# Optimization experiments

Hardware: AMD Instinct MI355X
Metric: run time of the kernel (lower is better)

## Reference

```python
import jax, jax.numpy as jnp
import numpy as np
import math

N_EMBD = 768
N_HEAD = 12
B, T = 4, 2048
HEAD_DIM = N_EMBD // N_HEAD


def new_gelu(x):
    # GPT-2 tanh approximation of GELU (NewGELUActivation)
    c = math.sqrt(2.0 / math.pi)
    return 0.5 * x * (1.0 + jnp.tanh(c * (x + 0.044715 * jnp.power(x, 3.0))))


def layer_norm(x, g, b, eps=1e-5):
    mu = jnp.mean(x, axis=-1, keepdims=True)
    var = jnp.mean(jnp.square(x - mu), axis=-1, keepdims=True)
    return (x - mu) * jax.lax.rsqrt(var + eps) * g + b


def setup_inputs() -> dict:
    key = jax.random.key(0)
    ks = jax.random.split(key, 12)
    s = 0.02
    return {
        "x": jax.random.normal(ks[0], (B, T, N_EMBD), dtype=jnp.float32),
        "ln1_g": jnp.ones((N_EMBD,), jnp.float32),
        "ln1_b": jnp.zeros((N_EMBD,), jnp.float32),
        "W_attn": jax.random.normal(ks[1], (N_EMBD, 3 * N_EMBD), jnp.float32) * s,
        "b_attn": jnp.zeros((3 * N_EMBD,), jnp.float32),
        "W_proj": jax.random.normal(ks[2], (N_EMBD, N_EMBD), jnp.float32) * s,
        "b_proj": jnp.zeros((N_EMBD,), jnp.float32),
        "ln2_g": jnp.ones((N_EMBD,), jnp.float32),
        "ln2_b": jnp.zeros((N_EMBD,), jnp.float32),
        "W_fc": jax.random.normal(ks[3], (N_EMBD, 4 * N_EMBD), jnp.float32) * s,
        "b_fc": jnp.zeros((4 * N_EMBD,), jnp.float32),
        "W_fc2": jax.random.normal(ks[4], (4 * N_EMBD, N_EMBD), jnp.float32) * s,
        "b_fc2": jnp.zeros((N_EMBD,), jnp.float32),
    }


def block_forward(x, ln1_g, ln1_b, W_attn, b_attn, W_proj, b_proj,
                  ln2_g, ln2_b, W_fc, b_fc, W_fc2, b_fc2):
    # ---- attention sublayer (pre-LN) ----
    h = layer_norm(x, ln1_g, ln1_b)
    qkv = h @ W_attn + b_attn                      # [B,T,3C]
    q, k, v = jnp.split(qkv, 3, axis=-1)
    q = q.reshape(B, T, N_HEAD, HEAD_DIM).transpose(0, 2, 1, 3)  # [B,H,T,D]
    k = k.reshape(B, T, N_HEAD, HEAD_DIM).transpose(0, 2, 1, 3)
    v = v.reshape(B, T, N_HEAD, HEAD_DIM).transpose(0, 2, 1, 3)
    scores = jnp.einsum('bhqd,bhkd->bhqk', q, k) / math.sqrt(HEAD_DIM)
    causal = jnp.tril(jnp.ones((T, T), dtype=bool))
    scores = jnp.where(causal[None, None, :, :], scores, -jnp.inf)
    attn = jax.nn.softmax(scores, axis=-1)
    y = jnp.einsum('bhqk,bhkd->bhqd', attn, v)      # [B,H,T,D]
    y = y.transpose(0, 2, 1, 3).reshape(B, T, N_EMBD)
    y = y @ W_proj + b_proj
    x = x + y
    # ---- MLP sublayer ----
    h = layer_norm(x, ln2_g, ln2_b)
    h = new_gelu(h @ W_fc + b_fc)
    h = h @ W_fc2 + b_fc2
    return x + h


def reference(x, ln1_g, ln1_b, W_attn, b_attn, W_proj, b_proj,
              ln2_g, ln2_b, W_fc, b_fc, W_fc2, b_fc2):
    return block_forward(x, ln1_g, ln1_b, W_attn, b_attn, W_proj, b_proj,
                         ln2_g, ln2_b, W_fc, b_fc, W_fc2, b_fc2)
```

## Files before the change

kernel.cpp:

```cpp
#include <hip/hip_runtime.h>
#include <hip/hip_bf16.h>

typedef __attribute__((ext_vector_type(8))) short short8;
typedef __attribute__((ext_vector_type(4))) float f32x4;
typedef __attribute__((ext_vector_type(8))) unsigned short u16x8;
typedef __attribute__((ext_vector_type(4))) unsigned short u16x4;

#define MFMA16(A, B, C) __builtin_amdgcn_mfma_f32_16x16x32_bf16(A, B, C, 0, 0, 0)

static __device__ __forceinline__ unsigned short f2bf(float f) {
    unsigned int u = __builtin_bit_cast(unsigned int, f);
    u += 0x7FFF + ((u >> 16) & 1);
    return (unsigned short)(u >> 16);
}

static __device__ __forceinline__ float bf2f(unsigned short u) {
    return __builtin_bit_cast(float, (unsigned int)u << 16);
}

static __device__ __forceinline__ unsigned int cvt_pk_bf16(float a, float b) {
    unsigned int r;
    asm("v_cvt_pk_bf16_f32 %0, %1, %2" : "=v"(r) : "v"(a), "v"(b));
    return r;
}

static __device__ __forceinline__ float gelu_f(float v) {
    const float k1 = 2.3022077646f;
    const float k2 = 0.1029432207f;
    float t = __builtin_amdgcn_exp2f(-(k1 * v + k2 * v * v * v));
    return v * __builtin_amdgcn_rcpf(1.0f + t);
}

typedef const __attribute__((address_space(1))) unsigned int* gas_t;
typedef __attribute__((address_space(3))) unsigned int* las_t;
static __device__ __forceinline__ void gl_lds16(const void* g, void* l) {
    __builtin_amdgcn_global_load_lds((gas_t)g, (las_t)l, 16, 0, 0);
}

__global__ __launch_bounds__(256)
void wtrans_all(const float* __restrict__ W0, const float* __restrict__ W1,
                const float* __restrict__ W2, const float* __restrict__ W3,
                unsigned short* __restrict__ T0, unsigned short* __restrict__ T1,
                unsigned short* __restrict__ T2, unsigned short* __restrict__ T3) {
    __shared__ float tl[32][33];
    const int idx = blockIdx.x;
    const float* W; unsigned short* Wt; int K, N, nx, bx;
    if (idx < 1728)      { W = W0; Wt = T0; K = 768;  N = 2304; bx = idx;        nx = 72; }
    else if (idx < 2304) { W = W1; Wt = T1; K = 768;  N = 768;  bx = idx - 1728; nx = 24; }
    else if (idx < 4608) { W = W2; Wt = T2; K = 768;  N = 3072; bx = idx - 2304; nx = 96; }
    else                 { W = W3; Wt = T3; K = 3072; N = 768;  bx = idx - 4608; nx = 24; }
    const int n0 = (bx % nx) * 32, k0 = (bx / nx) * 32;
    const int tx = threadIdx.x & 31, ty = threadIdx.x >> 5;
#pragma unroll
    for (int i = 0; i < 4; i++)
        tl[ty + 8 * i][tx] = W[(long)(k0 + ty + 8 * i) * N + n0 + tx];
    __syncthreads();
#pragma unroll
    for (int i = 0; i < 4; i++)
        Wt[(long)(n0 + ty + 8 * i) * K + k0 + tx] = f2bf(tl[tx][ty + 8 * i]);
}

template <bool BF16IN>
__global__ __launch_bounds__(256)
void ln_fwd(const void* __restrict__ xin, const float* __restrict__ gw,
            const float* __restrict__ bw, unsigned short* __restrict__ out) {
    const int row = blockIdx.x * 4 + (threadIdx.x >> 6);
    const int ln = threadIdx.x & 63;
    float4 v[3];
    if constexpr (BF16IN) {
        const unsigned short* xr = (const unsigned short*)xin + (long)row * 768;
#pragma unroll
        for (int j = 0; j < 3; j++) {
            u16x4 t = *(const u16x4*)(xr + (ln + 64 * j) * 4);
            v[j].x = bf2f(t[0]); v[j].y = bf2f(t[1]);
            v[j].z = bf2f(t[2]); v[j].w = bf2f(t[3]);
        }
    } else {
        const float4* xr = (const float4*)((const float*)xin + (long)row * 768);
#pragma unroll
        for (int j = 0; j < 3; j++) v[j] = xr[ln + 64 * j];
    }
    float s = 0.f;
#pragma unroll
    for (int j = 0; j < 3; j++) s += v[j].x + v[j].y + v[j].z + v[j].w;
#pragma unroll
    for (int off = 32; off >= 1; off >>= 1) s += __shfl_xor(s, off);
    const float mean = s * (1.0f / 768.0f);
    float sq = 0.f;
#pragma unroll
    for (int j = 0; j < 3; j++) {
        float a = v[j].x - mean, b = v[j].y - mean, c = v[j].z - mean, d = v[j].w - mean;
        sq += a * a + b * b + c * c + d * d;
    }
#pragma unroll
    for (int off = 32; off >= 1; off >>= 1) sq += __shfl_xor(sq, off);
    const float rstd = rsqrtf(sq * (1.0f / 768.0f) + 1e-5f);
#pragma unroll
    for (int j = 0; j < 3; j++) {
        const int c = ln + 64 * j;
        float4 gg = ((const float4*)gw)[c];
        float4 bb = ((const float4*)bw)[c];
        u16x4 o;
        o[0] = f2bf((v[j].x - mean) * rstd * gg.x + bb.x);
        o[1] = f2bf((v[j].y - mean) * rstd * gg.y + bb.y);
        o[2] = f2bf((v[j].z - mean) * rstd * gg.z + bb.z);
        o[3] = f2bf((v[j].w - mean) * rstd * gg.w + bb.w);
        *(u16x4*)(out + (long)row * 768 + c * 4) = o;
    }
}

template <int MODE, int BN, int BM, int BK>
__global__ __launch_bounds__(BM * 2)
void gemm_bt(const unsigned short* __restrict__ A, const unsigned short* __restrict__ Bt,
             const float* __restrict__ bias, const void* __restrict__ resid,
             void* __restrict__ Out, unsigned short* __restrict__ vT,
             int M, int N, int K) {
    constexpr int NTH = BM * 2;
    constexpr int NW = BN / 32;
    constexpr int CHK = BK / 8;
    constexpr int BUF = (BM + BN) * BK;
    constexpr int RPP = NTH / CHK;
    constexpr int RPW = 64 / CHK;
    constexpr int PA = BM / RPP;
    constexpr int PB = BN / RPP;
    constexpr int STN = (BN == 128) ? 132 : 68;
    constexpr int SEGS = NTH / 64;
    constexpr int CPT = BN / SEGS;
    constexpr int BYTES_MAIN = 2 * BUF * 2;
    constexpr int BYTES_ST = 64 * STN * 4;
    constexpr int BYTES = BYTES_MAIN > BYTES_ST ? BYTES_MAIN : BYTES_ST;
    __shared__ char smem[BYTES];
    unsigned short* ubase = (unsigned short*)smem;
    float* st = (float*)smem;

    const int tid = threadIdx.x;
    const int wv = tid >> 6, ln = tid & 63;
    const int wm = wv >> 1, wn = wv & 1;
    const int g = ln >> 4, r = ln & 15;
    const int sr = ln / CHK, sc = ln % CHK;
    const int ssw = (BK == 32) ? (sc ^ ((sr >> 1) & 3)) : (sc ^ (sr & 7));
    const long mbase = (long)blockIdx.x * BM;
    const long nbase = (long)blockIdx.y * BN;

    f32x4 acc[4][NW];
    const f32x4 zero = {0.f, 0.f, 0.f, 0.f};
#pragma unroll
    for (int m = 0; m < 4; m++)
#pragma unroll
        for (int n = 0; n < NW; n++) acc[m][n] = zero;

    const int nt = K / BK;
#pragma unroll
    for (int p = 0; p < PA; p++)
        gl_lds16(A + (mbase + p * RPP + wv * RPW + sr) * (long)K + ssw * 8,
                 ubase + (p * RPP + wv * RPW) * BK);
#pragma unroll
    for (int p = 0; p < PB; p++)
        gl_lds16(Bt + (nbase + p * RPP + wv * RPW + sr) * (long)K + ssw * 8,
                 ubase + BM * BK + (p * RPP + wv * RPW) * BK);
    __syncthreads();

    const int cx = (r >> 1) & 3;
    const int rx = r & 7;
    for (int t = 0; t < nt; t++) {
        const unsigned short* cbuf = ubase + (t & 1) * BUF;
        if (t + 1 < nt) {
            unsigned short* nbuf = ubase + ((t + 1) & 1) * BUF;
            const long k0 = (long)(t + 1) * BK;
#pragma unroll
            for (int p = 0; p < PA; p++)
                gl_lds16(A + (mbase + p * RPP + wv * RPW + sr) * (long)K + k0 + ssw * 8,
                         nbuf + (p * RPP + wv * RPW) * BK);
#pragma unroll
            for (int p = 0; p < PB; p++)
                gl_lds16(Bt + (nbase + p * RPP + wv * RPW + sr) * (long)K + k0 + ssw * 8,
                         nbuf + BM * BK + (p * RPP + wv * RPW) * BK);
        }
        if constexpr (BK == 32) {
            short8 af[4], bfr[NW];
#pragma unroll
            for (int m = 0; m < 4; m++)
                af[m] = *(const short8*)(cbuf + (wm * 64 + m * 16 + r) * 32 + ((g ^ cx) * 8));
#pragma unroll
            for (int n = 0; n < NW; n++)
                bfr[n] = *(const short8*)(cbuf + BM * 32 + (wn * (BN / 2) + n * 16 + r) * 32 + ((g ^ cx) * 8));
#pragma unroll
            for (int m = 0; m < 4; m++)
#pragma unroll
                for (int n = 0; n < NW; n++) acc[m][n] = MFMA16(af[m], bfr[n], acc[m][n]);
        } else {
#pragma unroll
            for (int ks = 0; ks < 2; ks++) {
                short8 af[4], bfr[NW];
#pragma unroll
                for (int m = 0; m < 4; m++)
                    af[m] = *(const short8*)(cbuf + (wm * 64 + m * 16 + r) * 64 + (((g + 4 * ks) ^ rx) * 8));
#pragma unroll
                for (int n = 0; n < NW; n++)
                    bfr[n] = *(const short8*)(cbuf + BM * 64 + (wn * (BN / 2) + n * 16 + r) * 64 + (((g + 4 * ks) ^ rx) * 8));
#pragma unroll
                for (int m = 0; m < 4; m++)
#pragma unroll
                    for (int n = 0; n < NW; n++) acc[m][n] = MFMA16(af[m], bfr[n], acc[m][n]);
            }
        }
        __syncthreads();
    }

    const int tr = tid / SEGS, seg = tid % SEGS;
#pragma unroll 1
    for (int half = 0; half < BM / 64; half++) {
        __syncthreads();
        if (wm == half) {
#pragma unroll
            for (int m = 0; m < 4; m++)
#pragma unroll
                for (int n = 0; n < NW; n++)
#pragma unroll
                    for (int i = 0; i < 4; i++)
                        st[(m * 16 + g * 4 + i) * STN + wn * (BN / 2) + n * 16 + r] = acc[m][n][i];
        }
        __syncthreads();
        const long row = mbase + half * 64 + tr;
        if constexpr (MODE == 1) {
            if (nbase >= 1536) {
                constexpr int DC = NTH / 8;
                const int tc = tid & 7;
                const int d0 = tid >> 3;
                const long bb = mbase >> 11;
                const int tg0 = (int)(mbase & 2047) + half * 64 + tc * 8;
#pragma unroll
                for (int it = 0; it < 128 / DC; it++) {
                    const int dl = it * DC + d0;
                    const int h = (int)((nbase - 1536) >> 6) + (dl >> 6);
                    const int dd = dl & 63;
                    const float bc = bias[nbase + dl];
                    u16x8 o;
#pragma unroll
                    for (int j = 0; j < 8; j++)
                        o[j] = f2bf(st[(tc * 8 + j) * STN + dl] + bc);
                    *(u16x8*)(vT + ((bb * 12 + h) * 64 + dd) * 2048 + tg0) = o;
                }
            } else {
                const float qs = (nbase < 768) ? 0.18033688011112042f : 1.0f;
                const long cb = nbase + seg * CPT;
                unsigned short* op = (unsigned short*)Out + row * N + cb;
#pragma unroll
                for (int u2 = 0; u2 < CPT / 8; u2++) {
                    float4 a = *(const float4*)(st + tr * STN + seg * CPT + u2 * 8);
                    float4 b = *(const float4*)(st + tr * STN + seg * CPT + u2 * 8 + 4);
                    float4 ba = ((const float4*)bias)[(cb >> 2) + u2 * 2];
                    float4 bb2 = ((const float4*)bias)[(cb >> 2) + u2 * 2 + 1];
                    a.x = (a.x + ba.x) * qs; a.y = (a.y + ba.y) * qs;
                    a.z = (a.z + ba.z) * qs; a.w = (a.w + ba.w) * qs;
                    b.x = (b.x + bb2.x) * qs; b.y = (b.y + bb2.y) * qs;
                    b.z = (b.z + bb2.z) * qs; b.w = (b.w + bb2.w) * qs;
                    uint4 w;
                    w.x = cvt_pk_bf16(a.x, a.y);
                    w.y = cvt_pk_bf16(a.z, a.w);
                    w.z = cvt_pk_bf16(b.x, b.y);
                    w.w = cvt_pk_bf16(b.z, b.w);
                    *(uint4*)(op + u2 * 8) = w;
                }
            }
        } else if constexpr (MODE == 3) {
            const long cb = nbase + seg * CPT;
            unsigned short* op = (unsigned short*)Out + row * N + cb;
#pragma unroll
            for (int u2 = 0; u2 < CPT / 8; u2++) {
                float4 a = *(const float4*)(st + tr * STN + seg * CPT + u2 * 8);
                float4 b = *(const float4*)(st + tr * STN + seg * CPT + u2 * 8 + 4);
                float4 ba = ((const float4*)bias)[(cb >> 2) + u2 * 2];
                float4 bb2 = ((const float4*)bias)[(cb >> 2) + u2 * 2 + 1];
                a.x = gelu_f(a.x + ba.x); a.y = gelu_f(a.y + ba.y);
                a.z = gelu_f(a.z + ba.z); a.w = gelu_f(a.w + ba.w);
                b.x = gelu_f(b.x + bb2.x); b.y = gelu_f(b.y + bb2.y);
                b.z = gelu_f(b.z + bb2.z); b.w = gelu_f(b.w + bb2.w);
                uint4 w;
                w.x = cvt_pk_bf16(a.x, a.y);
                w.y = cvt_pk_bf16(a.z, a.w);
                w.z = cvt_pk_bf16(b.x, b.y);
                w.w = cvt_pk_bf16(b.z, b.w);
                *(uint4*)(op + u2 * 8) = w;
            }
        } else if constexpr (MODE == 2) {
            const long cb = nbase + seg * CPT;
            unsigned short* op = (unsigned short*)Out + row * N + cb;
            const float* rp = (const float*)resid + row * N + cb;
#pragma unroll
            for (int u2 = 0; u2 < CPT / 8; u2++) {
                float4 a = *(const float4*)(st + tr * STN + seg * CPT + u2 * 8);
                float4 b = *(const float4*)(st + tr * STN + seg * CPT + u2 * 8 + 4);
                float4 ba = ((const float4*)bias)[(cb >> 2) + u2 * 2];
                float4 bb2 = ((const float4*)bias)[(cb >> 2) + u2 * 2 + 1];
                float4 ra = ((const float4*)rp)[u2 * 2];
                float4 rb = ((const float4*)rp)[u2 * 2 + 1];
                a.x += ba.x + ra.x; a.y += ba.y + ra.y;
                a.z += ba.z + ra.z; a.w += ba.w + ra.w;
                b.x += bb2.x + rb.x; b.y += bb2.y + rb.y;
                b.z += bb2.z + rb.z; b.w += bb2.w + rb.w;
                uint4 w;
                w.x = cvt_pk_bf16(a.x, a.y);
                w.y = cvt_pk_bf16(a.z, a.w);
                w.z = cvt_pk_bf16(b.x, b.y);
                w.w = cvt_pk_bf16(b.z, b.w);
                *(uint4*)(op + u2 * 8) = w;
            }
        } else {
            const long cb = nbase + seg * CPT;
            float* op = (float*)Out + row * N + cb;
            const unsigned short* rp = (const unsigned short*)resid + row * N + cb;
#pragma unroll
            for (int u = 0; u < CPT / 4; u++) {
                float4 a = *(const float4*)(st + tr * STN + seg * CPT + u * 4);
                float4 ba = ((const float4*)bias)[(cb >> 2) + u];
                u16x4 rv = *(const u16x4*)(rp + u * 4);
                a.x += ba.x + bf2f(rv[0]); a.y += ba.y + bf2f(rv[1]);
                a.z += ba.z + bf2f(rv[2]); a.w += ba.w + bf2f(rv[3]);
                ((float4*)op)[u] = a;
            }
        }
    }
}

__global__ __launch_bounds__(256)
void attn_fwd(const unsigned short* __restrict__ qkv, const unsigned short* __restrict__ vT,
              unsigned short* __restrict__ y) {
    const int pair = blockIdx.x;
    const int bh = blockIdx.y;
    const int b = bh / 12, h = bh % 12;
    const int qtA = pair, qtB = 31 - pair;
    __shared__ unsigned short smem[2 * 64 * 64 + 2 * 64 * 64 + 64 * 64];
    unsigned short* Kl = smem;
    unsigned short* Vl = smem + 2 * 4096;
    unsigned short* Pl = smem + 4 * 4096;
    const int tid = threadIdx.x;
    const int wv = tid >> 6, ln = tid & 63;
    const int g = ln >> 4, r = ln & 15;
    const int lr = ln >> 3, l8 = ln & 7;
    const int sw = l8 ^ lr;
    const int rx = r & 7;
    const f32x4 zero = {0.f, 0.f, 0.f, 0.f};
    const int q = wv * 16 + r;

    const int q7 = q & 7;
    unsigned short* plw[4];
#pragma unroll
    for (int kf = 0; kf < 4; kf++)
        plw[kf] = Pl + q * 64 + ((2 * kf + (g >> 1)) ^ q7) * 8 + (g & 1) * 4;
    const unsigned short* plr0 = Pl + q * 64 + (g ^ q7) * 8;
    const unsigned short* plr1 = Pl + q * 64 + ((4 + g) ^ q7) * 8;

    const long qoffA = ((long)(b * 2048 + qtA * 64 + q)) * 2304 + h * 64;
    const long qoffB = ((long)(b * 2048 + qtB * 64 + q)) * 2304 + h * 64;
    short8 bqA0 = *(const short8*)(qkv + qoffA + g * 8);
    short8 bqA1 = *(const short8*)(qkv + qoffA + 32 + g * 8);
    short8 bqB0 = *(const short8*)(qkv + qoffB + g * 8);
    short8 bqB1 = *(const short8*)(qkv + qoffB + 32 + g * 8);

    float lA = 0.0f, lB = 0.0f;
    f32x4 oA[4], oB[4];
#pragma unroll
    for (int f = 0; f < 4; f++) { oA[f] = zero; oB[f] = zero; }

    auto process = [&](const short8& b0, const short8& b1, float& lrow,
                       f32x4* oacc, bool diag, const unsigned short* Kb,
                       const unsigned short* Vb) {
        f32x4 s[4];
#pragma unroll
        for (int kf = 0; kf < 4; kf++) {
            short8 a0 = *(const short8*)(Kb + (kf * 16 + r) * 64 + (g ^ rx) * 8);
            short8 a1 = *(const short8*)(Kb + (kf * 16 + r) * 64 + ((g + 4) ^ rx) * 8);
            s[kf] = MFMA16(a0, b0, zero);
            s[kf] = MFMA16(a1, b1, s[kf]);
        }
        if (diag) {
#pragma unroll
            for (int kf = 0; kf < 4; kf++)
#pragma unroll
                for (int i = 0; i < 4; i++)
                    if (kf * 16 + g * 4 + i > q) s[kf][i] = -1e30f;
        }
        float pv[4][4];
        float psum = 0.f;
#pragma unroll
        for (int kf = 0; kf < 4; kf++)
#pragma unroll
            for (int i = 0; i < 4; i++) {
                pv[kf][i] = __builtin_amdgcn_exp2f(s[kf][i]);
                psum += pv[kf][i];
            }
        psum += __shfl_xor(psum, 16);
        psum += __shfl_xor(psum, 32);
        lrow += psum;
#pragma unroll
        for (int kf = 0; kf < 4; kf++) {
            uint2 w;
            w.x = cvt_pk_bf16(pv[kf][0], pv[kf][1]);
            w.y = cvt_pk_bf16(pv[kf][2], pv[kf][3]);
            *(uint2*)plw[kf] = w;
        }
        short8 pb0 = *(const short8*)plr0;
        short8 pb1 = *(const short8*)plr1;
#pragma unroll
        for (int f = 0; f < 4; f++) {
            short8 va0 = *(const short8*)(Vb + (f * 16 + r) * 64 + (g ^ rx) * 8);
            short8 va1 = *(const short8*)(Vb + (f * 16 + r) * 64 + ((g + 4) ^ rx) * 8);
            oacc[f] = MFMA16(va0, pb0, oacc[f]);
            oacc[f] = MFMA16(va1, pb1, oacc[f]);
        }
    };

#pragma unroll
    for (int p = 0; p < 2; p++) {
        const int row = wv * 8 + p * 32 + lr;
        gl_lds16(qkv + ((long)(b * 2048 + row)) * 2304 + 768 + h * 64 + sw * 8,
                 (char*)Kl + (wv * 8 + p * 32) * 128);
        gl_lds16(vT + ((long)(bh * 64 + row)) * 2048 + sw * 8,
                 (char*)Vl + (wv * 8 + p * 32) * 128);
    }
    __syncthreads();

    for (int kt = 0; kt <= qtB; ++kt) {
        const unsigned short* Kb = Kl + (kt & 1) * 4096;
        const unsigned short* Vb = Vl + (kt & 1) * 4096;
        if (kt < qtB) {
            char* Kn = (char*)Kl + ((kt + 1) & 1) * 8192;
            char* Vn = (char*)Vl + ((kt + 1) & 1) * 8192;
#pragma unroll
            for (int p = 0; p < 2; p++) {
                const int row = wv * 8 + p * 32 + lr;
                gl_lds16(qkv + ((long)(b * 2048 + (kt + 1) * 64 + row)) * 2304 + 768 + h * 64 + sw * 8,
                         Kn + (wv * 8 + p * 32) * 128);
                gl_lds16(vT + ((long)(bh * 64 + row)) * 2048 + (kt + 1) * 64 + sw * 8,
                         Vn + (wv * 8 + p * 32) * 128);
            }
        }
        if (kt <= qtA) process(bqA0, bqA1, lA, oA, kt == qtA, Kb, Vb);
        process(bqB0, bqB1, lB, oB, kt == qtB, Kb, Vb);
        __syncthreads();
    }

#pragma unroll 1
    for (int e = 0; e < 2; e++) {
        const float inv = 1.0f / (e ? lB : lA);
        const f32x4* oacc = e ? oB : oA;
        const int q0 = (e ? qtB : qtA) * 64;
#pragma unroll
        for (int f = 0; f < 4; f++) {
            uint2 w;
            w.x = cvt_pk_bf16(oacc[f][0] * inv, oacc[f][1] * inv);
            w.y = cvt_pk_bf16(oacc[f][2] * inv, oacc[f][3] * inv);
            *(uint2*)plw[f] = w;
        }
        __syncthreads();
#pragma unroll
        for (int p = 0; p < 2; p++) {
            int idx = p * 256 + tid;
            int row = idx >> 3, cc = idx & 7;
            *(u16x8*)(y + ((long)(b * 2048 + q0 + row)) * 768 + h * 64 + cc * 8) =
                *(const u16x8*)(Pl + row * 64 + (cc ^ (row & 7)) * 8);
        }
        __syncthreads();
    }
}

extern "C" void kernel_launch(void* const* d_in, const int* in_sizes, int n_in,
                              void* d_out, int out_size, void* d_ws, size_t ws_size,
                              hipStream_t stream) {
    const float* x      = (const float*)d_in[0];
    const float* ln1_g  = (const float*)d_in[1];
    const float* ln1_b  = (const float*)d_in[2];
    const float* W_attn = (const float*)d_in[3];
    const float* b_attn = (const float*)d_in[4];
    const float* W_proj = (const float*)d_in[5];
    const float* b_proj = (const float*)d_in[6];
    const float* ln2_g  = (const float*)d_in[7];
    const float* ln2_b  = (const float*)d_in[8];
    const float* W_fc   = (const float*)d_in[9];
    const float* b_fc   = (const float*)d_in[10];
    const float* W_fc2  = (const float*)d_in[11];
    const float* b_fc2  = (const float*)d_in[12];

    char* ws = (char*)d_ws;
    size_t off = 0;
    auto alloc = [&](size_t bytes) -> char* {
        char* p = ws + off;
        off += (bytes + 255) & ~(size_t)255;
        return p;
    };
    unsigned short* WtA  = (unsigned short*)alloc((size_t)2304 * 768 * 2);
    unsigned short* WtP  = (unsigned short*)alloc((size_t)768 * 768 * 2);
    unsigned short* WtF  = (unsigned short*)alloc((size_t)3072 * 768 * 2);
    unsigned short* WtF2 = (unsigned short*)alloc((size_t)768 * 3072 * 2);
    unsigned short* bigA = (unsigned short*)alloc((size_t)8192 * 3072 * 2);
    unsigned short* x1   = (unsigned short*)alloc((size_t)8192 * 768 * 2);
    unsigned short* bufD = (unsigned short*)alloc((size_t)8192 * 768 * 2);
    unsigned short* vT   = (unsigned short*)alloc((size_t)48 * 64 * 2048 * 2);

    wtrans_all<<<6912, 256, 0, stream>>>(W_attn, W_proj, W_fc, W_fc2, WtA, WtP, WtF, WtF2);
    ln_fwd<false><<<2048, 256, 0, stream>>>(x, ln1_g, ln1_b, bufD);
    gemm_bt<1, 128, 256, 32><<<dim3(32, 18), 512, 0, stream>>>(bufD, WtA, b_attn, nullptr, bigA, vT, 8192, 2304, 768);
    attn_fwd<<<dim3(16, 48), 256, 0, stream>>>(bigA, vT, bufD);
    gemm_bt<2, 64, 128, 64><<<dim3(64, 12), 256, 0, stream>>>(bufD, WtP, b_proj, x, x1, nullptr, 8192, 768, 768);
    ln_fwd<true><<<2048, 256, 0, stream>>>(x1, ln2_g, ln2_b, bufD);
    gemm_bt<3, 128, 256, 32><<<dim3(32, 24), 512, 0, stream>>>(bufD, WtF, b_fc, nullptr, bigA, nullptr, 8192, 3072, 768);
    gemm_bt<4, 64, 128, 64><<<dim3(64, 12), 256, 0, stream>>>(bigA, WtF2, b_fc2, x1, (float*)d_out, nullptr, 8192, 768, 3072);
}
```

Before: 246.5 us.

## Fuse weight transpose with first LayerNorm and store K in per-head contiguous layout

```diff
diff --git a/kernel.cpp b/kernel.cpp
--- a/kernel.cpp
+++ b/kernel.cpp
@@ -38,47 +38,79 @@
 }
 
 __global__ __launch_bounds__(256)
-void wtrans_all(const float* __restrict__ W0, const float* __restrict__ W1,
-                const float* __restrict__ W2, const float* __restrict__ W3,
-                unsigned short* __restrict__ T0, unsigned short* __restrict__ T1,
-                unsigned short* __restrict__ T2, unsigned short* __restrict__ T3) {
+void prep_all(const float* __restrict__ W0, const float* __restrict__ W1,
+              const float* __restrict__ W2, const float* __restrict__ W3,
+              unsigned short* __restrict__ T0, unsigned short* __restrict__ T1,
+              unsigned short* __restrict__ T2, unsigned short* __restrict__ T3,
+              const float* __restrict__ x, const float* __restrict__ gw,
+              const float* __restrict__ bw, unsigned short* __restrict__ lnout) {
     __shared__ float tl[32][33];
     const int idx = blockIdx.x;
-    const float* W; unsigned short* Wt; int K, N, nx, bx;
-    if (idx < 1728)      { W = W0; Wt = T0; K = 768;  N = 2304; bx = idx;        nx = 72; }
-    else if (idx < 2304) { W = W1; Wt = T1; K = 768;  N = 768;  bx = idx - 1728; nx = 24; }
-    else if (idx < 4608) { W = W2; Wt = T2; K = 768;  N = 3072; bx = idx - 2304; nx = 96; }
-    else                 { W = W3; Wt = T3; K = 3072; N = 768;  bx = idx - 4608; nx = 24; }
-    const int n0 = (bx % nx) * 32, k0 = (bx / nx) * 32;
-    const int tx = threadIdx.x & 31, ty = threadIdx.x >> 5;
-#pragma unroll
-    for (int i = 0; i < 4; i++)
-        tl[ty + 8 * i][tx] = W[(long)(k0 + ty + 8 * i) * N + n0 + tx];
-    __syncthreads();
-#pragma unroll
-    for (int i = 0; i < 4; i++)
-        Wt[(long)(n0 + ty + 8 * i) * K + k0 + tx] = f2bf(tl[tx][ty + 8 * i]);
-}
-
-template <bool BF16IN>
+    if (idx < 6912) {
+        const float* W; unsigned short* Wt; int K, N, nx, bx;
+        if (idx < 1728)      { W = W0; Wt = T0; K = 768;  N = 2304; bx = idx;        nx = 72; }
+        else if (idx < 2304) { W = W1; Wt = T1; K = 768;  N = 768;  bx = idx - 1728; nx = 24; }
+        else if (idx < 4608) { W = W2; Wt = T2; K = 768;  N = 3072; bx = idx - 2304; nx = 96; }
+        else                 { W = W3; Wt = T3; K = 3072; N = 768;  bx = idx - 4608; nx = 24; }
+        const int n0 = (bx % nx) * 32, k0 = (bx / nx) * 32;
+        const int tx = threadIdx.x & 31, ty = threadIdx.x >> 5;
+#pragma unroll
+        for (int i = 0; i < 4; i++)
+            tl[ty + 8 * i][tx] = W[(long)(k0 + ty + 8 * i) * N + n0 + tx];
+        __syncthreads();
+#pragma unroll
+        for (int i = 0; i < 4; i++)
+            Wt[(long)(n0 + ty + 8 * i) * K + k0 + tx] = f2bf(tl[tx][ty + 8 * i]);
+    } else {
+        const int row = (idx - 6912) * 4 + (threadIdx.x >> 6);
+        const int ln = threadIdx.x & 63;
+        const float4* xr = (const float4*)(x + (long)row * 768);
+        float4 v[3];
+        float s = 0.f;
+#pragma unroll
+        for (int j = 0; j < 3; j++) {
+            v[j] = xr[ln + 64 * j];
+            s += v[j].x + v[j].y + v[j].z + v[j].w;
+        }
+#pragma unroll
+        for (int off = 32; off >= 1; off >>= 1) s += __shfl_xor(s, off);
+        const float mean = s * (1.0f / 768.0f);
+        float sq = 0.f;
+#pragma unroll
+        for (int j = 0; j < 3; j++) {
+            float a = v[j].x - mean, b = v[j].y - mean, c = v[j].z - mean, d = v[j].w - mean;
+            sq += a * a + b * b + c * c + d * d;
+        }
+#pragma unroll
+        for (int off = 32; off >= 1; off >>= 1) sq += __shfl_xor(sq, off);
+        const float rstd = rsqrtf(sq * (1.0f / 768.0f) + 1e-5f);
+#pragma unroll
+        for (int j = 0; j < 3; j++) {
+            const int c = ln + 64 * j;
+            float4 gg = ((const float4*)gw)[c];
+            float4 bb = ((const float4*)bw)[c];
+            u16x4 o;
+            o[0] = f2bf((v[j].x - mean) * rstd * gg.x + bb.x);
+            o[1] = f2bf((v[j].y - mean) * rstd * gg.y + bb.y);
+            o[2] = f2bf((v[j].z - mean) * rstd * gg.z + bb.z);
+            o[3] = f2bf((v[j].w - mean) * rstd * gg.w + bb.w);
+            *(u16x4*)(lnout + (long)row * 768 + c * 4) = o;
+        }
+    }
+}
+
 __global__ __launch_bounds__(256)
-void ln_fwd(const void* __restrict__ xin, const float* __restrict__ gw,
-            const float* __restrict__ bw, unsigned short* __restrict__ out) {
+void ln_fwd_bf16(const unsigned short* __restrict__ xin, const float* __restrict__ gw,
+                 const float* __restrict__ bw, unsigned short* __restrict__ out) {
     const int row = blockIdx.x * 4 + (threadIdx.x >> 6);
     const int ln = threadIdx.x & 63;
+    const unsigned short* xr = xin + (long)row * 768;
     float4 v[3];
-    if constexpr (BF16IN) {
-        const unsigned short* xr = (const unsigned short*)xin + (long)row * 768;
-#pragma unroll
-        for (int j = 0; j < 3; j++) {
-            u16x4 t = *(const u16x4*)(xr + (ln + 64 * j) * 4);
-            v[j].x = bf2f(t[0]); v[j].y = bf2f(t[1]);
-            v[j].z = bf2f(t[2]); v[j].w = bf2f(t[3]);
-        }
-    } else {
-        const float4* xr = (const float4*)((const float*)xin + (long)row * 768);
-#pragma unroll
-        for (int j = 0; j < 3; j++) v[j] = xr[ln + 64 * j];
+#pragma unroll
+    for (int j = 0; j < 3; j++) {
+        u16x4 t = *(const u16x4*)(xr + (ln + 64 * j) * 4);
+        v[j].x = bf2f(t[0]); v[j].y = bf2f(t[1]);
+        v[j].z = bf2f(t[2]); v[j].w = bf2f(t[3]);
     }
     float s = 0.f;
 #pragma unroll
@@ -114,7 +146,7 @@
 void gemm_bt(const unsigned short* __restrict__ A, const unsigned short* __restrict__ Bt,
              const float* __restrict__ bias, const void* __restrict__ resid,
              void* __restrict__ Out, unsigned short* __restrict__ vT,
-             int M, int N, int K) {
+             unsigned short* __restrict__ kP, int M, int N, int K) {
     constexpr int NTH = BM * 2;
     constexpr int NW = BN / 32;
     constexpr int CHK = BK / 8;
@@ -241,8 +273,29 @@
                         o[j] = f2bf(st[(tc * 8 + j) * STN + dl] + bc);
                     *(u16x8*)(vT + ((bb * 12 + h) * 64 + dd) * 2048 + tg0) = o;
                 }
+            } else if (nbase >= 768) {
+                const long cb = nbase + seg * CPT;
+                const long bb = row >> 11;
+                const int t = (int)(row & 2047);
+#pragma unroll
+                for (int u2 = 0; u2 < CPT / 8; u2++) {
+                    const int dcol = (int)(cb - 768) + u2 * 8;
+                    const int hh = dcol >> 6, dd = dcol & 63;
+                    float4 a = *(const float4*)(st + tr * STN + seg * CPT + u2 * 8);
+                    float4 b = *(const float4*)(st + tr * STN + seg * CPT + u2 * 8 + 4);
+                    float4 ba = ((const float4*)bias)[(cb >> 2) + u2 * 2];
+                    float4 bb2 = ((const float4*)bias)[(cb >> 2) + u2 * 2 + 1];
+                    a.x += ba.x; a.y += ba.y; a.z += ba.z; a.w += ba.w;
+                    b.x += bb2.x; b.y += bb2.y; b.z += bb2.z; b.w += bb2.w;
+                    uint4 w;
+                    w.x = cvt_pk_bf16(a.x, a.y);
+                    w.y = cvt_pk_bf16(a.z, a.w);
+                    w.z = cvt_pk_bf16(b.x, b.y);
+                    w.w = cvt_pk_bf16(b.z, b.w);
+                    *(uint4*)(kP + ((bb * 12 + hh) * 2048 + t) * 64 + dd) = w;
+                }
             } else {
-                const float qs = (nbase < 768) ? 0.18033688011112042f : 1.0f;
+                const float qs = 0.18033688011112042f;
                 const long cb = nbase + seg * CPT;
                 unsigned short* op = (unsigned short*)Out + row * N + cb;
 #pragma unroll
@@ -325,7 +378,7 @@
 
 __global__ __launch_bounds__(256)
 void attn_fwd(const unsigned short* __restrict__ qkv, const unsigned short* __restrict__ vT,
-              unsigned short* __restrict__ y) {
+              const unsigned short* __restrict__ kP, unsigned short* __restrict__ y) {
     const int pair = blockIdx.x;
     const int bh = blockIdx.y;
     const int b = bh / 12, h = bh % 12;
@@ -363,6 +416,8 @@
 #pragma unroll
     for (int f = 0; f < 4; f++) { oA[f] = zero; oB[f] = zero; }
 
+    const long kbase = (long)bh * 2048;
+
     auto process = [&](const short8& b0, const short8& b1, float& lrow,
                        f32x4* oacc, bool diag, const unsigned short* Kb,
                        const unsigned short* Vb) {
@@ -414,7 +469,7 @@
 #pragma unroll
     for (int p = 0; p < 2; p++) {
         const int row = wv * 8 + p * 32 + lr;
-        gl_lds16(qkv + ((long)(b * 2048 + row)) * 2304 + 768 + h * 64 + sw * 8,
+        gl_lds16(kP + (kbase + row) * 64 + sw * 8,
                  (char*)Kl + (wv * 8 + p * 32) * 128);
         gl_lds16(vT + ((long)(bh * 64 + row)) * 2048 + sw * 8,
                  (char*)Vl + (wv * 8 + p * 32) * 128);
@@ -430,7 +485,7 @@
 #pragma unroll
             for (int p = 0; p < 2; p++) {
                 const int row = wv * 8 + p * 32 + lr;
-                gl_lds16(qkv + ((long)(b * 2048 + (kt + 1) * 64 + row)) * 2304 + 768 + h * 64 + sw * 8,
+                gl_lds16(kP + (kbase + (kt + 1) * 64 + row) * 64 + sw * 8,
                          Kn + (wv * 8 + p * 32) * 128);
                 gl_lds16(vT + ((long)(bh * 64 + row)) * 2048 + (kt + 1) * 64 + sw * 8,
                          Vn + (wv * 8 + p * 32) * 128);
@@ -497,13 +552,14 @@
     unsigned short* x1   = (unsigned short*)alloc((size_t)8192 * 768 * 2);
     unsigned short* bufD = (unsigned short*)alloc((size_t)8192 * 768 * 2);
     unsigned short* vT   = (unsigned short*)alloc((size_t)48 * 64 * 2048 * 2);
-
-    wtrans_all<<<6912, 256, 0, stream>>>(W_attn, W_proj, W_fc, W_fc2, WtA, WtP, WtF, WtF2);
-    ln_fwd<false><<<2048, 256, 0, stream>>>(x, ln1_g, ln1_b, bufD);
-    gemm_bt<1, 128, 256, 32><<<dim3(32, 18), 512, 0, stream>>>(bufD, WtA, b_attn, nullptr, bigA, vT, 8192, 2304, 768);
-    attn_fwd<<<dim3(16, 48), 256, 0, stream>>>(bigA, vT, bufD);
-    gemm_bt<2, 64, 128, 64><<<dim3(64, 12), 256, 0, stream>>>(bufD, WtP, b_proj, x, x1, nullptr, 8192, 768, 768);
-    ln_fwd<true><<<2048, 256, 0, stream>>>(x1, ln2_g, ln2_b, bufD);
-    gemm_bt<3, 128, 256, 32><<<dim3(32, 24), 512, 0, stream>>>(bufD, WtF, b_fc, nullptr, bigA, nullptr, 8192, 3072, 768);
-    gemm_bt<4, 64, 128, 64><<<dim3(64, 12), 256, 0, stream>>>(bigA, WtF2, b_fc2, x1, (float*)d_out, nullptr, 8192, 768, 3072);
-}
+    unsigned short* kP   = bigA + (size_t)8192 * 2304;
+
+    prep_all<<<8960, 256, 0, stream>>>(W_attn, W_proj, W_fc, W_fc2, WtA, WtP, WtF, WtF2,
+                                       x, ln1_g, ln1_b, bufD);
+    gemm_bt<1, 128, 256, 32><<<dim3(32, 18), 512, 0, stream>>>(bufD, WtA, b_attn, nullptr, bigA, vT, kP, 8192, 2304, 768);
+    attn_fwd<<<dim3(16, 48), 256, 0, stream>>>(bigA, vT, kP, bufD);
+    gemm_bt<2, 64, 128, 64><<<dim3(64, 12), 256, 0, stream>>>(bufD, WtP, b_proj, x, x1, nullptr, nullptr, 8192, 768, 768);
+    ln_fwd_bf16<<<2048, 256, 0, stream>>>(x1, ln2_g, ln2_b, bufD);
+    gemm_bt<3, 128, 256, 32><<<dim3(32, 24), 512, 0, stream>>>(bufD, WtF, b_fc, nullptr, bigA, nullptr, nullptr, 8192, 3072, 768);
+    gemm_bt<4, 64, 128, 64><<<dim3(64, 12), 256, 0, stream>>>(bigA, WtF2, b_fc2, x1, (float*)d_out, nullptr, nullptr, 8192, 768, 3072);
+}
```

New measurement: 255.6 us. 1.04x slower.
